# Optimization experiments

Hardware: AMD Instinct MI355X
Metric: run time of the kernel (lower is better)

The kernel has to match this reference:

```python
import jax, jax.numpy as jnp
import numpy as np

GAMMA = 0.99
RHO_THRESHOLD = 1.0
C_THRESHOLD = 1.0
BASELINE_LOSS_SCALING = 0.5
ENT_COEFF = 0.01
PPO_CLIP = 0.2


def setup_inputs() -> dict:
    key = jax.random.key(0)
    ks = jax.random.split(key, 7)
    T, B, A = 512, 8192, 2
    return {
        "prob": jax.random.uniform(ks[0], (T, B, A), dtype=jnp.float32),
        "action_prob": jax.random.uniform(ks[1], (T, B, A), dtype=jnp.float32),
        "v": jax.random.normal(ks[2], (T, B), dtype=jnp.float32),
        "next_v": jax.random.normal(ks[3], (T, B), dtype=jnp.float32),
        "reward": jax.random.normal(ks[4], (T, B), dtype=jnp.float32),
        "action": jax.random.randint(ks[5], (T, B), 0, 2, dtype=jnp.int32),
        "done": jax.random.randint(ks[6], (T, B), 0, 2, dtype=jnp.int32),
    }


def _log_prob(p, a):
    # torch.distributions.Categorical normalizes unnormalized probs
    logp = jnp.log(p) - jnp.log(p.sum(-1, keepdims=True))  # [T,B,A]
    return jnp.take_along_axis(logp, a[..., None].astype(jnp.int32), axis=-1)[..., 0]


def reference(prob, action_prob, v, next_v, reward, action, done):
    done_f = done.astype(v.dtype)  # [T,B]
    logp = _log_prob(prob, action)
    logp_act = _log_prob(action_prob, action)
    ratio = jnp.exp(logp - logp_act)  # [T,B]

    clipped_rho = jnp.minimum(ratio, RHO_THRESHOLD)
    clipped_c = jnp.minimum(ratio, C_THRESHOLD)
    deltas = clipped_rho * (reward + (1.0 - done_f) * GAMMA * next_v - v)

    # V-trace backward recurrence over time (dim 0), vectorized over batch
    def step(next_vtrace, xs):
        v_t, d_t, c_t, rho_t, r_t, nv_t, dn_t = xs
        vt = v_t + d_t + GAMMA * c_t * (next_vtrace - nv_t) * (1.0 - dn_t)
        adv = rho_t * (r_t + GAMMA * next_vtrace * (1.0 - dn_t) - v_t)
        return vt, (vt, adv)

    _, (vtrace, adv) = jax.lax.scan(
        step, next_v[-1],
        (v, deltas, clipped_c, clipped_rho, reward, next_v, done_f),
        reverse=True)

    vtrace = jax.lax.stop_gradient(vtrace)  # .detach() in original
    adv = jax.lax.stop_gradient(adv)

    critic_loss = BASELINE_LOSS_SCALING * jnp.mean((v - vtrace) ** 2)
    surr1 = ratio * adv
    surr2 = jnp.clip(ratio, 1.0 - PPO_CLIP, 1.0 + PPO_CLIP) * adv
    actor_loss = -jnp.minimum(surr1, surr2).mean()

    # entropy is logged but NOT included in total_loss in the original
    total_loss = actor_loss + critic_loss
    return total_loss
```

## Files before the change

### kernel.cpp

```cpp
#include <hip/hip_runtime.h>

#define T_DIM 512
#define B_DIM 8192
#define GB 16
#define NC 32
#define LC 16
#define GAMMA 0.99f

__launch_bounds__(512, 4)
__global__ void vtrace_main(const float* __restrict__ prob,
                            const float* __restrict__ aprob,
                            const float* __restrict__ v,
                            const float* __restrict__ nv,
                            const float* __restrict__ rw,
                            const int* __restrict__ act,
                            const int* __restrict__ dnn,
                            float* __restrict__ partials) {
    __shared__ float Sc[NC][GB];
    __shared__ float Mc[NC][GB];
    __shared__ float Cin[NC][GB];
    __shared__ float red[16];

    const int tid = threadIdx.x;
    const int bl  = tid & (GB - 1);
    const int c   = tid >> 4;
    const int b   = blockIdx.x * GB + bl;
    const int t0  = c * LC;

    float rat[LC], mm[LC], pp[LC], ss[LC];
    float S = 0.0f, M = 1.0f;

    const float2* __restrict__ prob2  = (const float2*)prob;
    const float2* __restrict__ aprob2 = (const float2*)aprob;

#pragma unroll
    for (int i = LC - 1; i >= 0; --i) {
        const size_t idx = (size_t)(t0 + i) * B_DIM + b;
        float2 pr = prob2[idx];
        float2 qr = aprob2[idx];
        float vv  = v[idx];
        float nvv = nv[idx];
        float rr  = rw[idx];
        int   a   = act[idx];
        int   d   = dnn[idx];

        float pa    = a ? pr.y : pr.x;
        float qa    = a ? qr.y : qr.x;
        float ratio = (pa * (qr.x + qr.y)) / ((pr.x + pr.y) * qa);
        float rho   = fminf(ratio, 1.0f);
        float m     = d ? 0.0f : GAMMA * rho;
        float p     = rho * (rr - vv);
        (void)nvv;

        rat[i] = ratio; mm[i] = m; pp[i] = p; ss[i] = vv + p;
        S = ss[i] + m * S;
        M = m * M;
    }

    Sc[c][bl] = S;
    Mc[c][bl] = M;
    __syncthreads();

    if (tid < GB) {
        float carry = nv[(size_t)(T_DIM - 1) * B_DIM + blockIdx.x * GB + tid];
        for (int cc = NC - 1; cc >= 0; --cc) {
            Cin[cc][tid] = carry;
            carry = Sc[cc][tid] + Mc[cc][tid] * carry;
        }
    }
    __syncthreads();

    float carry  = Cin[c][bl];
    float critic = 0.0f, msum = 0.0f;
#pragma unroll
    for (int i = LC - 1; i >= 0; --i) {
        float adv = pp[i] + mm[i] * carry;
        carry     = ss[i] + mm[i] * carry;
        critic += adv * adv;
        float r_ = rat[i];
        float rc = fminf(fmaxf(r_, 0.8f), 1.2f);
        msum += fminf(r_ * adv, rc * adv);
    }

#pragma unroll
    for (int off = 32; off > 0; off >>= 1) {
        critic += __shfl_down(critic, off, 64);
        msum   += __shfl_down(msum, off, 64);
    }
    const int wave = tid >> 6;
    if ((tid & 63) == 0) { red[wave] = critic; red[8 + wave] = msum; }
    __syncthreads();
    if (tid == 0) {
        float cs = 0.0f, ms = 0.0f;
#pragma unroll
        for (int w = 0; w < 8; ++w) { cs += red[w]; ms += red[8 + w]; }
        partials[blockIdx.x]       = cs;
        partials[512 + blockIdx.x] = ms;
    }
}

__global__ void vtrace_final(const float* __restrict__ partials,
                             float* __restrict__ out) {
    __shared__ float red[16];
    const int tid = threadIdx.x;
    float cs = partials[tid];
    float ms = partials[512 + tid];
#pragma unroll
    for (int off = 32; off > 0; off >>= 1) {
        cs += __shfl_down(cs, off, 64);
        ms += __shfl_down(ms, off, 64);
    }
    const int wave = tid >> 6;
    if ((tid & 63) == 0) { red[wave] = cs; red[8 + wave] = ms; }
    __syncthreads();
    if (tid == 0) {
        float c = 0.0f, m = 0.0f;
#pragma unroll
        for (int w = 0; w < 8; ++w) { c += red[w]; m += red[8 + w]; }
        const float invN = 1.0f / (float)((size_t)T_DIM * B_DIM);
        out[0] = 0.5f * c * invN - m * invN;
    }
}

extern "C" void kernel_launch(void* const* d_in, const int* in_sizes, int n_in,
                              void* d_out, int out_size, void* d_ws, size_t ws_size,
                              hipStream_t stream) {
    const float* prob  = (const float*)d_in[0];
    const float* aprob = (const float*)d_in[1];
    const float* v     = (const float*)d_in[2];
    const float* nv    = (const float*)d_in[3];
    const float* rw    = (const float*)d_in[4];
    const int*   act   = (const int*)d_in[5];
    const int*   dnn   = (const int*)d_in[6];
    float* partials = (float*)d_ws;
    float* out      = (float*)d_out;

    vtrace_main<<<B_DIM / GB, GB * NC, 0, stream>>>(prob, aprob, v, nv, rw,
                                                    act, dnn, partials);
    vtrace_final<<<1, 512, 0, stream>>>(partials, out);
}
```

Baseline: 169.9 us.

## Fuse final reduction via atomics, double chunk count, compact per-step state

```diff
diff --git a/kernel.cpp b/kernel.cpp
--- a/kernel.cpp
+++ b/kernel.cpp
@@ -3,11 +3,13 @@
 #define T_DIM 512
 #define B_DIM 8192
 #define GB 16
-#define NC 32
-#define LC 16
+#define NC 64
+#define LC 8
+#define BLOCK (GB * NC)
+#define GRID (B_DIM / GB)
 #define GAMMA 0.99f
 
-__launch_bounds__(512, 4)
+__launch_bounds__(BLOCK, 8)
 __global__ void vtrace_main(const float* __restrict__ prob,
                             const float* __restrict__ aprob,
                             const float* __restrict__ v,
@@ -15,11 +17,12 @@
                             const float* __restrict__ rw,
                             const int* __restrict__ act,
                             const int* __restrict__ dnn,
-                            float* __restrict__ partials) {
+                            float* __restrict__ ws,
+                            float* __restrict__ out) {
     __shared__ float Sc[NC][GB];
     __shared__ float Mc[NC][GB];
     __shared__ float Cin[NC][GB];
-    __shared__ float red[16];
+    __shared__ float red[32];
 
     const int tid = threadIdx.x;
     const int bl  = tid & (GB - 1);
@@ -27,7 +30,7 @@
     const int b   = blockIdx.x * GB + bl;
     const int t0  = c * LC;
 
-    float rat[LC], mm[LC], pp[LC], ss[LC];
+    float rsA[LC], pA[LC], vA[LC];
     float S = 0.0f, M = 1.0f;
 
     const float2* __restrict__ prob2  = (const float2*)prob;
@@ -39,7 +42,6 @@
         float2 pr = prob2[idx];
         float2 qr = aprob2[idx];
         float vv  = v[idx];
-        float nvv = nv[idx];
         float rr  = rw[idx];
         int   a   = act[idx];
         int   d   = dnn[idx];
@@ -50,10 +52,11 @@
         float rho   = fminf(ratio, 1.0f);
         float m     = d ? 0.0f : GAMMA * rho;
         float p     = rho * (rr - vv);
-        (void)nvv;
 
-        rat[i] = ratio; mm[i] = m; pp[i] = p; ss[i] = vv + p;
-        S = ss[i] + m * S;
+        rsA[i] = d ? -ratio : ratio;
+        pA[i]  = p;
+        vA[i]  = vv;
+        S = (vv + p) + m * S;
         M = m * M;
     }
 
@@ -74,10 +77,12 @@
     float critic = 0.0f, msum = 0.0f;
 #pragma unroll
     for (int i = LC - 1; i >= 0; --i) {
-        float adv = pp[i] + mm[i] * carry;
-        carry     = ss[i] + mm[i] * carry;
+        float rs  = rsA[i];
+        float r_  = fabsf(rs);
+        float m   = (rs > 0.0f) ? GAMMA * fminf(r_, 1.0f) : 0.0f;
+        float adv = pA[i] + m * carry;
+        carry     = adv + vA[i];
         critic += adv * adv;
-        float r_ = rat[i];
         float rc = fminf(fmaxf(r_, 0.8f), 1.2f);
         msum += fminf(r_ * adv, rc * adv);
     }
@@ -88,37 +93,25 @@
         msum   += __shfl_down(msum, off, 64);
     }
     const int wave = tid >> 6;
-    if ((tid & 63) == 0) { red[wave] = critic; red[8 + wave] = msum; }
+    if ((tid & 63) == 0) { red[wave] = critic; red[16 + wave] = msum; }
     __syncthreads();
+
     if (tid == 0) {
         float cs = 0.0f, ms = 0.0f;
 #pragma unroll
-        for (int w = 0; w < 8; ++w) { cs += red[w]; ms += red[8 + w]; }
-        partials[blockIdx.x]       = cs;
-        partials[512 + blockIdx.x] = ms;
-    }
-}
-
-__global__ void vtrace_final(const float* __restrict__ partials,
-                             float* __restrict__ out) {
-    __shared__ float red[16];
-    const int tid = threadIdx.x;
-    float cs = partials[tid];
-    float ms = partials[512 + tid];
-#pragma unroll
-    for (int off = 32; off > 0; off >>= 1) {
-        cs += __shfl_down(cs, off, 64);
-        ms += __shfl_down(ms, off, 64);
-    }
-    const int wave = tid >> 6;
-    if ((tid & 63) == 0) { red[wave] = cs; red[8 + wave] = ms; }
-    __syncthreads();
-    if (tid == 0) {
-        float c = 0.0f, m = 0.0f;
-#pragma unroll
-        for (int w = 0; w < 8; ++w) { c += red[w]; m += red[8 + w]; }
-        const float invN = 1.0f / (float)((size_t)T_DIM * B_DIM);
-        out[0] = 0.5f * c * invN - m * invN;
+        for (int w = 0; w < 16; ++w) { cs += red[w]; ms += red[16 + w]; }
+        atomicAdd(&ws[0], cs);
+        atomicAdd(&ws[1], ms);
+        __threadfence();
+        unsigned* cnt = (unsigned*)(ws + 2);
+        unsigned ticket = atomicAdd(cnt, 1u);
+        if (ticket == GRID - 1) {
+            __threadfence();
+            float c_tot = atomicAdd(&ws[0], 0.0f);
+            float m_tot = atomicAdd(&ws[1], 0.0f);
+            const float invN = 1.0f / (float)((size_t)T_DIM * B_DIM);
+            out[0] = 0.5f * c_tot * invN - m_tot * invN;
+        }
     }
 }
 
@@ -132,10 +125,10 @@
     const float* rw    = (const float*)d_in[4];
     const int*   act   = (const int*)d_in[5];
     const int*   dnn   = (const int*)d_in[6];
-    float* partials = (float*)d_ws;
-    float* out      = (float*)d_out;
+    float* ws  = (float*)d_ws;
+    float* out = (float*)d_out;
 
-    vtrace_main<<<B_DIM / GB, GB * NC, 0, stream>>>(prob, aprob, v, nv, rw,
-                                                    act, dnn, partials);
-    vtrace_final<<<1, 512, 0, stream>>>(partials, out);
+    hipMemsetAsync(ws, 0, 12, stream);
+    vtrace_main<<<GRID, BLOCK, 0, stream>>>(prob, aprob, v, nv, rw, act, dnn,
+                                            ws, out);
 }
```

Result: slower. 189.3 us (+11.4%).
